# Kernel tuning notes

Hardware: AMD Instinct MI355X
Metric: run time of the kernel (lower is better)

Reference implementation:

```python
import jax, jax.numpy as jnp
import numpy as np

B, S, HID = 4, 1024, 1024
H = 16
D = HID // H  # 64
SPARSITY = 0.9  # keep prob = 0.1


def setup_inputs() -> dict:
    key = jax.random.key(0)
    ks = jax.random.split(key, 11)
    sc = 1.0 / np.sqrt(HID)
    x = jax.random.normal(ks[0], (B, S, HID), dtype=jnp.float32)
    Wq = jax.random.normal(ks[1], (HID, HID), dtype=jnp.float32) * sc
    bq = jnp.zeros((HID,), dtype=jnp.float32)
    Wk = jax.random.normal(ks[2], (HID, HID), dtype=jnp.float32) * sc
    bk = jnp.zeros((HID,), dtype=jnp.float32)
    Wv = jax.random.normal(ks[3], (HID, HID), dtype=jnp.float32) * sc
    bv = jnp.zeros((HID,), dtype=jnp.float32)
    Wo = jax.random.normal(ks[4], (HID, HID), dtype=jnp.float32) * sc
    bo = jnp.zeros((HID,), dtype=jnp.float32)
    temperature = jnp.ones((H, 1, 1), dtype=jnp.float32)
    # training-mode random sparsity mask: rand > sparsity -> keep (True)
    sparse_mask = jax.random.uniform(ks[5], (B, H, S, S)) > SPARSITY
    return {"x": x, "Wq": Wq, "bq": bq, "Wk": Wk, "bk": bk, "Wv": Wv,
            "bv": bv, "Wo": Wo, "bo": bo, "temperature": temperature,
            "sparse_mask": sparse_mask}


def reference(x, Wq, bq, Wk, bk, Wv, bv, Wo, bo, temperature, sparse_mask):
    b, s, _ = x.shape
    def split_heads(t):
        return t.reshape(b, s, H, D).transpose(0, 2, 1, 3)  # [B,H,S,D]
    q = split_heads(x @ Wq + bq)
    k = split_heads(x @ Wk + bk)
    v = split_heads(x @ Wv + bv)
    scores = jnp.einsum('bhqd,bhkd->bhqk', q, k) / np.sqrt(D)
    scores = scores * temperature  # [H,1,1] broadcasts over [B,H,S,S]
    scores = jnp.where(sparse_mask, scores, -jnp.inf)
    attn = jax.nn.softmax(scores, axis=-1)
    out = jnp.einsum('bhqk,bhkd->bhqd', attn, v)
    out = out.transpose(0, 2, 1, 3).reshape(b, s, HID)
    return out @ Wo + bo
```

## Files before the change

### kernel.cpp

```cpp
#include <hip/hip_runtime.h>

typedef unsigned short u16;
typedef short short8 __attribute__((ext_vector_type(8)));
typedef float f32x4 __attribute__((ext_vector_type(4)));
typedef float float4v __attribute__((ext_vector_type(4)));
typedef u16 u16x4 __attribute__((ext_vector_type(4)));
typedef unsigned uint2v __attribute__((ext_vector_type(2)));
typedef unsigned long long u64;

__device__ __forceinline__ u16 f2bf(float f) {
  union { float f; unsigned u; } v; v.f = f;
  unsigned r = v.u + 0x7FFFu + ((v.u >> 16) & 1u);
  return (u16)(r >> 16);
}

__device__ __forceinline__ unsigned cvtpk(float lo, float hi) {
  unsigned r;
  asm("v_cvt_pk_bf16_f32 %0, %1, %2" : "=v"(r) : "v"(lo), "v"(hi));
  return r;
}

__device__ __forceinline__ void gload16(const void* g, void* l) {
  __builtin_amdgcn_global_load_lds(
      (const __attribute__((address_space(1))) void*)g,
      (__attribute__((address_space(3))) void*)l, 16, 0, 0);
}

union PackSS { unsigned u[4]; short8 s; };

__global__ __launch_bounds__(256)
void cvt_kernel(const float* __restrict__ x, u16* __restrict__ xb,
                const float* __restrict__ W0, const float* __restrict__ W1,
                const float* __restrict__ W2, const float* __restrict__ W3,
                u16* __restrict__ Wt) {
  __shared__ float t[32][33];
  const int bid = blockIdx.x;
  if (bid < 4096) {
    int i = (bid * 256 + threadIdx.x) * 4;
    float4v v = *(const float4v*)(x + i);
    u16x4 o;
    o[0] = f2bf(v[0]); o[1] = f2bf(v[1]); o[2] = f2bf(v[2]); o[3] = f2bf(v[3]);
    *(u16x4*)(xb + i) = o;
  } else {
    int i = bid - 4096;
    int z = i >> 10, rest = i & 1023;
    const float* W = (z == 0) ? W0 : (z == 1) ? W1 : (z == 2) ? W2 : W3;
    u16* outw = Wt + (size_t)z * 1048576;
    int n0 = (rest & 31) * 32, k0 = (rest >> 5) * 32;
    int tx = threadIdx.x & 31, ty = threadIdx.x >> 5;
#pragma unroll
    for (int j = 0; j < 4; ++j)
      t[ty + 8 * j][tx] = W[(size_t)(k0 + ty + 8 * j) * 1024 + n0 + tx];
    __syncthreads();
#pragma unroll
    for (int j = 0; j < 4; ++j)
      outw[(size_t)(n0 + ty + 8 * j) * 1024 + k0 + tx] = f2bf(t[tx][ty + 8 * j]);
  }
}

template<int BM, int BN>
__global__ __launch_bounds__(256, 3)
void gemm_kernel(const u16* __restrict__ A,
                 const u16* __restrict__ Bt0, const u16* __restrict__ Bt1, const u16* __restrict__ Bt2,
                 const float* __restrict__ b0, const float* __restrict__ b1, const float* __restrict__ b2,
                 const float* __restrict__ temp,
                 u16* __restrict__ qb, u16* __restrict__ kb, u16* __restrict__ vT,
                 float* __restrict__ fo, int phase,
                 const void* __restrict__ mask, u64* __restrict__ bits) {
  constexpr int K = 1024;
  constexpr int WM = BM / 2;
  constexpr int WN = BN / 2;
  constexpr int MR = WM / 16;
  constexpr int NC = WN / 16;
  __shared__ u16 As[BM * 32];
  __shared__ u16 Bs[BN * 32];
  __shared__ int sf;
  const int tid = threadIdx.x;
  const int lane = tid & 63, w = tid >> 6;
  const int l15 = lane & 15, l4 = lane >> 4;
  const int m0 = blockIdx.x * BM, n0 = blockIdx.y * BN;
  const int z = blockIdx.z;
  const u16* Bt = (z == 0) ? Bt0 : (z == 1) ? Bt1 : Bt2;
  const float* bias = (z == 0) ? b0 : (z == 1) ? b1 : b2;
  const int wr = w >> 1, wc = w & 1;

  f32x4 acc[MR][NC] = {};

  const int c0 = tid, c1 = 256 + tid;
  const u16* ga0 = A + (size_t)(m0 + (c0 >> 2)) * K + (c0 & 3) * 8;
  const u16* ga1 = A + (size_t)(m0 + (c1 >> 2)) * K + (c1 & 3) * 8;
  const u16* gb0 = Bt + (size_t)(n0 + (c0 >> 2)) * K + (c0 & 3) * 8;
  const u16* gb1 = Bt + (size_t)(n0 + (c1 >> 2)) * K + (c1 & 3) * 8;
  u16* la0 = As + c0 * 8;
  u16* la1 = As + c1 * 8;
  u16* lb0 = Bs + c0 * 8;
  u16* lb1 = Bs + c1 * 8;

  for (int kt = 0; kt < K; kt += 32) {
    gload16(ga0 + kt, la0);
    if (BM == 128) gload16(ga1 + kt, la1);
    gload16(gb0 + kt, lb0);
    if (BN == 128) gload16(gb1 + kt, lb1);
    __syncthreads();
    short8 af[MR], bfr[NC];
#pragma unroll
    for (int r = 0; r < MR; ++r)
      af[r] = *(const short8*)(As + (wr * WM + r * 16 + l15) * 32 + l4 * 8);
#pragma unroll
    for (int c = 0; c < NC; ++c)
      bfr[c] = *(const short8*)(Bs + (wc * WN + c * 16 + l15) * 32 + l4 * 8);
#pragma unroll
    for (int r = 0; r < MR; ++r)
#pragma unroll
      for (int c = 0; c < NC; ++c)
        acc[r][c] = __builtin_amdgcn_mfma_f32_16x16x32_bf16(bfr[c], af[r], acc[r][c], 0, 0, 0);
    __syncthreads();
  }

  float bvj[NC][4];
#pragma unroll
  for (int c = 0; c < NC; ++c)
#pragma unroll
    for (int j = 0; j < 4; ++j)
      bvj[c][j] = bias[n0 + wc * WN + c * 16 + l4 * 4 + j];
  const float fac = (phase == 0 && z == 0)
      ? temp[(n0 + wc * WN) >> 6] * 0.18033688011112042f : 1.0f;

#pragma unroll
  for (int r = 0; r < MR; ++r) {
    const int mm = m0 + wr * WM + r * 16 + l15;
    const int b = mm >> 10, s = mm & 1023;
#pragma unroll
    for (int c = 0; c < NC; ++c) {
      const int n = n0 + wc * WN + c * 16 + l4 * 4;
      if (phase == 1) {
        float4v o;
#pragma unroll
        for (int j = 0; j < 4; ++j) o[j] = acc[r][c][j] + bvj[c][j];
        *(float4v*)(fo + (size_t)mm * 1024 + n) = o;
      } else if (z == 2) {
#pragma unroll
        for (int j = 0; j < 4; ++j)
          vT[((size_t)b * 1024 + n + j) * 1024 + s] = f2bf(acc[r][c][j] + bvj[c][j]);
      } else {
        unsigned lo = cvtpk((acc[r][c][0] + bvj[c][0]) * fac, (acc[r][c][1] + bvj[c][1]) * fac);
        unsigned hi = cvtpk((acc[r][c][2] + bvj[c][2]) * fac, (acc[r][c][3] + bvj[c][3]) * fac);
        unsigned o2[2] = {lo, hi};
        int hh = n >> 6, d = n & 63;
        u16* dst = (z == 0) ? qb : kb;
        *(unsigned long long*)(dst + ((((size_t)b * 16 + hh) * 1024 + s) * 64 + d)) =
            *(unsigned long long*)o2;
      }
    }
  }

  if (phase == 0) {
    if (tid == 0) sf = 0;
    __syncthreads();
    {
      uint4 v = ((const uint4*)mask)[tid];
      unsigned xs[4] = {v.x, v.y, v.z, v.w};
      int f = 0;
#pragma unroll
      for (int d = 0; d < 4; ++d) {
        unsigned u = xs[d];
        if (u == 0x3F800000u) f |= 1;
        if (u & 0xFFFFFF00u) f |= 2;
        if ((d & 1) && u) f |= 4;
      }
      if (f) atomicOr(&sf, f);
    }
    __syncthreads();
    const int fl = sf;
    const int fmt = (fl & 1) ? 2 : ((fl & 2) ? 0 : ((fl & 4) ? 1 : 3));

    const int gb = z * 256 + blockIdx.y * 32 + blockIdx.x;
    for (int it = 0; it < 6; ++it) {
      const int wi = (it * 768 + gb) * 256 + tid;
      if (wi >= 1048576) break;
      u64 b = 0;
      if (fmt == 0) {
        const uint4* mp = (const uint4*)mask + (size_t)wi * 4;
#pragma unroll
        for (int i = 0; i < 4; ++i) {
          uint4 v = mp[i];
          unsigned xw[4] = {v.x, v.y, v.z, v.w};
#pragma unroll
          for (int d = 0; d < 4; ++d)
#pragma unroll
            for (int by = 0; by < 4; ++by)
              if (xw[d] & (0xFFu << (by * 8))) b |= 1ULL << (i * 16 + d * 4 + by);
        }
      } else if (fmt != 3) {
        const uint4* mp = (const uint4*)mask + (size_t)wi * 16;
#pragma unroll
        for (int i = 0; i < 16; ++i) {
          uint4 v = mp[i];
          if (v.x) b |= 1ULL << (i * 4 + 0);
          if (v.y) b |= 1ULL << (i * 4 + 1);
          if (v.z) b |= 1ULL << (i * 4 + 2);
          if (v.w) b |= 1ULL << (i * 4 + 3);
        }
      } else {
        const uint4* mp = (const uint4*)mask + (size_t)wi * 32;
#pragma unroll
        for (int i = 0; i < 32; ++i) {
          uint4 v = mp[i];
          if (v.x | v.y) b |= 1ULL << (i * 2 + 0);
          if (v.z | v.w) b |= 1ULL << (i * 2 + 1);
        }
      }
      int bh = wi >> 14, q = (wi >> 4) & 1023, kt = wi & 15;
      bits[((size_t)bh * 16 + kt) * 1024 + q] = b;
    }
  }
}

__device__ __forceinline__ void softmax_reg(f32x4* s, u64 wcur, float& m,
                                            f32x4* oacc, f32x4& lacc, int l4,
                                            PackSS& p0, PackSS& p1) {
  float mt = fmaxf(fmaxf(s[0][0], s[0][1]), fmaxf(s[0][2], s[0][3]));
#pragma unroll
  for (int cb = 1; cb < 4; ++cb)
    mt = fmaxf(mt, fmaxf(fmaxf(s[cb][0], s[cb][1]), fmaxf(s[cb][2], s[cb][3])));
  mt = fmaxf(mt, __shfl_xor(mt, 16));
  mt = fmaxf(mt, __shfl_xor(mt, 32));
  if (!__all(mt <= m + 8.f)) {
    float mnew = fmaxf(m, mt);
    float al = exp2f(m - mnew);
    lacc *= al;
#pragma unroll
    for (int db = 0; db < 4; ++db) oacc[db] *= al;
    m = mnew;
  }
  unsigned hws[4] = {(unsigned)wcur, (unsigned)(wcur >> 16),
                     (unsigned)(wcur >> 32), (unsigned)(wcur >> 48)};
#pragma unroll
  for (int cb = 0; cb < 4; ++cb) {
#pragma unroll
    for (int j = 0; j < 4; ++j) {
      float p = exp2f(s[cb][j] - m);
      s[cb][j] = ((hws[cb] >> (l4 * 4 + j)) & 1) ? p : 0.f;
    }
  }
  p0.u[0] = cvtpk(s[0][0], s[0][1]); p0.u[1] = cvtpk(s[0][2], s[0][3]);
  p0.u[2] = cvtpk(s[1][0], s[1][1]); p0.u[3] = cvtpk(s[1][2], s[1][3]);
  p1.u[0] = cvtpk(s[2][0], s[2][1]); p1.u[1] = cvtpk(s[2][2], s[2][3]);
  p1.u[2] = cvtpk(s[3][0], s[3][1]); p1.u[3] = cvtpk(s[3][2], s[3][3]);
}

__global__ __launch_bounds__(256, 3)
void attn_kernel(const u16* __restrict__ qb, const u16* __restrict__ kb,
                 const u16* __restrict__ vT, const u64* __restrict__ mbits,
                 u16* __restrict__ oh) {
  __shared__ u16 Ks[2][64 * 64];
  __shared__ u16 Vs[2][64 * 64];
  const int tid = threadIdx.x, lane = tid & 63, w = tid >> 6;
  const int l15 = lane & 15, l4 = lane >> 4;
  const int id = blockIdx.x;
  const int xcd = id & 7;
  const int bh = xcd * 8 + ((id >> 3) & 7), qx = id >> 6;
  const int b = bh >> 4, h = bh & 15;
  const int q0 = qx * 128 + w * 32;
  const u16* qp = qb + ((size_t)bh * 1024 + q0) * 64;
  const u16* kp = kb + (size_t)bh * 1024 * 64;
  const u16* vp = vT + (size_t)bh * 64 * 1024;

  const int L0 = tid, L1 = tid + 256;
  const int r0 = L0 >> 3, c0 = ((L0 & 7) ^ (r0 & 7)) * 8;
  const int r1 = L1 >> 3, c1 = ((L1 & 7) ^ (r1 & 7)) * 8;
  const int swz8 = (l15 & 7) << 3;
  const int vswz = l15 & 7;

  int koff[4], vr[4], ke0, ke1, ve[2][2];
#pragma unroll
  for (int cb = 0; cb < 4; ++cb) koff[cb] = (cb * 16 + l15) * 64;
#pragma unroll
  for (int db = 0; db < 4; ++db) vr[db] = (db * 16 + l15) * 64;
  ke0 = (l4 * 8) ^ swz8;
  ke1 = (32 + l4 * 8) ^ swz8;
#pragma unroll
  for (int kg = 0; kg < 2; ++kg) {
    ve[kg][0] = (((4 * kg + (l4 >> 1)) ^ vswz) << 3) + (l4 & 1) * 4;
    ve[kg][1] = (((4 * kg + 2 + (l4 >> 1)) ^ vswz) << 3) + (l4 & 1) * 4;
  }

  short8 qa0 = *(const short8*)(qp + (size_t)l15 * 64 + l4 * 8);
  short8 qa1 = *(const short8*)(qp + (size_t)l15 * 64 + 32 + l4 * 8);
  short8 qb0 = *(const short8*)(qp + (size_t)(16 + l15) * 64 + l4 * 8);
  short8 qb1 = *(const short8*)(qp + (size_t)(16 + l15) * 64 + 32 + l4 * 8);

  PackSS ones;
  ones.u[0] = 0x3F803F80u; ones.u[1] = 0x3F803F80u;
  ones.u[2] = 0x3F803F80u; ones.u[3] = 0x3F803F80u;

  float mA = -1e30f, mB = -1e30f;
  f32x4 oA[4] = {}, oB[4] = {};
  f32x4 lA4 = {}, lB4 = {};

  const u64* mb = mbits + (size_t)bh * 16 * 1024 + q0 + l15;
  u64 wA = mb[0], wB = mb[16];

  gload16(kp + (size_t)r0 * 64 + c0, &Ks[0][L0 * 8]);
  gload16(kp + (size_t)r1 * 64 + c1, &Ks[0][L1 * 8]);
  gload16(vp + (size_t)r0 * 1024 + c0, &Vs[0][L0 * 8]);
  gload16(vp + (size_t)r1 * 1024 + c1, &Vs[0][L1 * 8]);

  for (int t = 0; t < 16; ++t) {
    const int buf = t & 1;
    __syncthreads();

    if (t < 15) {
      const int k1 = (t + 1) * 64;
      gload16(kp + (size_t)(k1 + r0) * 64 + c0, &Ks[buf ^ 1][L0 * 8]);
      gload16(kp + (size_t)(k1 + r1) * 64 + c1, &Ks[buf ^ 1][L1 * 8]);
      gload16(vp + (size_t)r0 * 1024 + k1 + c0, &Vs[buf ^ 1][L0 * 8]);
      gload16(vp + (size_t)r1 * 1024 + k1 + c1, &Vs[buf ^ 1][L1 * 8]);
    }
    u64 wAn = 0, wBn = 0;
    if (t < 15) { wAn = mb[(t + 1) * 1024]; wBn = mb[(t + 1) * 1024 + 16]; }

    const u16* kbase = Ks[buf];
    f32x4 sa[4] = {}, sb[4] = {};
    __builtin_amdgcn_s_setprio(1);
#pragma unroll
    for (int cb = 0; cb < 4; ++cb) {
      short8 kf0 = *(const short8*)(kbase + koff[cb] + ke0);
      short8 kf1 = *(const short8*)(kbase + koff[cb] + ke1);
      sa[cb] = __builtin_amdgcn_mfma_f32_16x16x32_bf16(kf0, qa0, sa[cb], 0, 0, 0);
      sa[cb] = __builtin_amdgcn_mfma_f32_16x16x32_bf16(kf1, qa1, sa[cb], 0, 0, 0);
      sb[cb] = __builtin_amdgcn_mfma_f32_16x16x32_bf16(kf0, qb0, sb[cb], 0, 0, 0);
      sb[cb] = __builtin_amdgcn_mfma_f32_16x16x32_bf16(kf1, qb1, sb[cb], 0, 0, 0);
    }
    __builtin_amdgcn_s_setprio(0);

    PackSS pa0, pa1, pb0, pb1;
    softmax_reg(sa, wA, mA, oA, lA4, l4, pa0, pa1);
    softmax_reg(sb, wB, mB, oB, lB4, l4, pb0, pb1);

    const u16* vbase = Vs[buf];
    __builtin_amdgcn_s_setprio(1);
#pragma unroll
    for (int kg = 0; kg < 2; ++kg) {
#pragma unroll
      for (int db = 0; db < 4; ++db) {
        uint2v v0 = *(const uint2v*)(vbase + vr[db] + ve[kg][0]);
        uint2v v1 = *(const uint2v*)(vbase + vr[db] + ve[kg][1]);
        PackSS vf;
        vf.u[0] = v0[0]; vf.u[1] = v0[1]; vf.u[2] = v1[0]; vf.u[3] = v1[1];
        oA[db] = __builtin_amdgcn_mfma_f32_16x16x32_bf16(
            vf.s, kg ? pa1.s : pa0.s, oA[db], 0, 0, 0);
        oB[db] = __builtin_amdgcn_mfma_f32_16x16x32_bf16(
            vf.s, kg ? pb1.s : pb0.s, oB[db], 0, 0, 0);
      }
      lA4 = __builtin_amdgcn_mfma_f32_16x16x32_bf16(
          ones.s, kg ? pa1.s : pa0.s, lA4, 0, 0, 0);
      lB4 = __builtin_amdgcn_mfma_f32_16x16x32_bf16(
          ones.s, kg ? pb1.s : pb0.s, lB4, 0, 0, 0);
    }
    __builtin_amdgcn_s_setprio(0);
    wA = wAn; wB = wBn;
  }

  float rlA = 1.f / lA4[0], rlB = 1.f / lB4[0];
  u16* orowA = oh + ((size_t)b * 1024 + q0 + l15) * 1024 + h * 64;
  u16* orowB = oh + ((size_t)b * 1024 + q0 + 16 + l15) * 1024 + h * 64;
#pragma unroll
  for (int db = 0; db < 4; ++db) {
    unsigned a0 = cvtpk(oA[db][0] * rlA, oA[db][1] * rlA);
    unsigned a1 = cvtpk(oA[db][2] * rlA, oA[db][3] * rlA);
    unsigned b0 = cvtpk(oB[db][0] * rlB, oB[db][1] * rlB);
    unsigned b1 = cvtpk(oB[db][2] * rlB, oB[db][3] * rlB);
    unsigned oAa[2] = {a0, a1}, oBb[2] = {b0, b1};
    *(unsigned long long*)(orowA + db * 16 + l4 * 4) = *(unsigned long long*)oAa;
    *(unsigned long long*)(orowB + db * 16 + l4 * 4) = *(unsigned long long*)oBb;
  }
}

extern "C" void kernel_launch(void* const* d_in, const int* in_sizes, int n_in,
                              void* d_out, int out_size, void* d_ws, size_t ws_size,
                              hipStream_t stream) {
  const float* x = (const float*)d_in[0];
  const float* Wq = (const float*)d_in[1];
  const float* bq = (const float*)d_in[2];
  const float* Wk = (const float*)d_in[3];
  const float* bk = (const float*)d_in[4];
  const float* Wv = (const float*)d_in[5];
  const float* bv = (const float*)d_in[6];
  const float* Wo = (const float*)d_in[7];
  const float* bo = (const float*)d_in[8];
  const float* temp = (const float*)d_in[9];
  const void* mask = (const void*)d_in[10];

  char* ws = (char*)d_ws;
  u16* xb = (u16*)(ws + 256);
  u16* Wt = xb + (size_t)4 * 1024 * 1024;
  u16* qbuf = Wt + (size_t)4 * 1024 * 1024;
  u16* kbuf = qbuf + (size_t)4 * 1024 * 1024;
  u16* vTb = kbuf + (size_t)4 * 1024 * 1024;
  u64* mbits = (u64*)(vTb + (size_t)4 * 1024 * 1024);
  u16* oh = xb;

  cvt_kernel<<<8192, 256, 0, stream>>>(x, xb, Wq, Wk, Wv, Wo, Wt);
  gemm_kernel<128, 128><<<dim3(32, 8, 3), 256, 0, stream>>>(
      xb, Wt, Wt + 1048576, Wt + 2 * 1048576,
      bq, bk, bv, temp, qbuf, kbuf, vTb, nullptr, 0, mask, mbits);
  attn_kernel<<<512, 256, 0, stream>>>(qbuf, kbuf, vTb, mbits, oh);
  gemm_kernel<64, 64><<<dim3(64, 16, 1), 256, 0, stream>>>(
      oh, Wt + 3 * 1048576, nullptr, nullptr,
      bo, nullptr, nullptr, temp, nullptr, nullptr, nullptr,
      (float*)d_out, 1, nullptr, nullptr);
}
```

Measured before the change: 164.4 us.

## Stagger two query sub-tiles' softmax and PV MFMAs, preload K/V fragments into registers

The inner loop now loads all K and V fragments from LDS into registers up front. It then interleaves work across the two 16-row query sub-tiles: softmax for A, PV for A, softmax for B, PV for B. This is meant to let the VALU-heavy softmax of one sub-tile overlap with the MFMA work of the other, and to hide LDS latency. Holding the extra fragments raises register pressure, so launch bounds drop from 3 to 2 blocks per SM, trading occupancy for instruction-level overlap.

```diff
diff --git a/kernel.cpp b/kernel.cpp
--- a/kernel.cpp
+++ b/kernel.cpp
@@ -249,7 +249,7 @@
   p1.u[2] = cvtpk(s[3][0], s[3][1]); p1.u[3] = cvtpk(s[3][2], s[3][3]);
 }
 
-__global__ __launch_bounds__(256, 3)
+__global__ __launch_bounds__(256, 2)
 void attn_kernel(const u16* __restrict__ qb, const u16* __restrict__ kb,
                  const u16* __restrict__ vT, const u64* __restrict__ mbits,
                  u16* __restrict__ oh) {
@@ -321,40 +321,64 @@
     if (t < 15) { wAn = mb[(t + 1) * 1024]; wBn = mb[(t + 1) * 1024 + 16]; }
 
     const u16* kbase = Ks[buf];
+    short8 kfr[8];
+#pragma unroll
+    for (int cb = 0; cb < 4; ++cb) {
+      kfr[2 * cb]     = *(const short8*)(kbase + koff[cb] + ke0);
+      kfr[2 * cb + 1] = *(const short8*)(kbase + koff[cb] + ke1);
+    }
+
     f32x4 sa[4] = {}, sb[4] = {};
     __builtin_amdgcn_s_setprio(1);
 #pragma unroll
     for (int cb = 0; cb < 4; ++cb) {
-      short8 kf0 = *(const short8*)(kbase + koff[cb] + ke0);
-      short8 kf1 = *(const short8*)(kbase + koff[cb] + ke1);
-      sa[cb] = __builtin_amdgcn_mfma_f32_16x16x32_bf16(kf0, qa0, sa[cb], 0, 0, 0);
-      sa[cb] = __builtin_amdgcn_mfma_f32_16x16x32_bf16(kf1, qa1, sa[cb], 0, 0, 0);
-      sb[cb] = __builtin_amdgcn_mfma_f32_16x16x32_bf16(kf0, qb0, sb[cb], 0, 0, 0);
-      sb[cb] = __builtin_amdgcn_mfma_f32_16x16x32_bf16(kf1, qb1, sb[cb], 0, 0, 0);
+      sa[cb] = __builtin_amdgcn_mfma_f32_16x16x32_bf16(kfr[2 * cb], qa0, sa[cb], 0, 0, 0);
+      sa[cb] = __builtin_amdgcn_mfma_f32_16x16x32_bf16(kfr[2 * cb + 1], qa1, sa[cb], 0, 0, 0);
+    }
+#pragma unroll
+    for (int cb = 0; cb < 4; ++cb) {
+      sb[cb] = __builtin_amdgcn_mfma_f32_16x16x32_bf16(kfr[2 * cb], qb0, sb[cb], 0, 0, 0);
+      sb[cb] = __builtin_amdgcn_mfma_f32_16x16x32_bf16(kfr[2 * cb + 1], qb1, sb[cb], 0, 0, 0);
     }
     __builtin_amdgcn_s_setprio(0);
 
-    PackSS pa0, pa1, pb0, pb1;
+    PackSS pa0, pa1;
     softmax_reg(sa, wA, mA, oA, lA4, l4, pa0, pa1);
-    softmax_reg(sb, wB, mB, oB, lB4, l4, pb0, pb1);
 
     const u16* vbase = Vs[buf];
-    __builtin_amdgcn_s_setprio(1);
-#pragma unroll
-    for (int kg = 0; kg < 2; ++kg) {
+    PackSS vfr[2][4];
+#pragma unroll
+    for (int kg = 0; kg < 2; ++kg)
 #pragma unroll
       for (int db = 0; db < 4; ++db) {
         uint2v v0 = *(const uint2v*)(vbase + vr[db] + ve[kg][0]);
         uint2v v1 = *(const uint2v*)(vbase + vr[db] + ve[kg][1]);
-        PackSS vf;
-        vf.u[0] = v0[0]; vf.u[1] = v0[1]; vf.u[2] = v1[0]; vf.u[3] = v1[1];
+        vfr[kg][db].u[0] = v0[0]; vfr[kg][db].u[1] = v0[1];
+        vfr[kg][db].u[2] = v1[0]; vfr[kg][db].u[3] = v1[1];
+      }
+
+    __builtin_amdgcn_s_setprio(1);
+#pragma unroll
+    for (int kg = 0; kg < 2; ++kg) {
+#pragma unroll
+      for (int db = 0; db < 4; ++db)
         oA[db] = __builtin_amdgcn_mfma_f32_16x16x32_bf16(
-            vf.s, kg ? pa1.s : pa0.s, oA[db], 0, 0, 0);
-        oB[db] = __builtin_amdgcn_mfma_f32_16x16x32_bf16(
-            vf.s, kg ? pb1.s : pb0.s, oB[db], 0, 0, 0);
-      }
+            vfr[kg][db].s, kg ? pa1.s : pa0.s, oA[db], 0, 0, 0);
       lA4 = __builtin_amdgcn_mfma_f32_16x16x32_bf16(
           ones.s, kg ? pa1.s : pa0.s, lA4, 0, 0, 0);
+    }
+    __builtin_amdgcn_s_setprio(0);
+
+    PackSS pb0, pb1;
+    softmax_reg(sb, wB, mB, oB, lB4, l4, pb0, pb1);
+
+    __builtin_amdgcn_s_setprio(1);
+#pragma unroll
+    for (int kg = 0; kg < 2; ++kg) {
+#pragma unroll
+      for (int db = 0; db < 4; ++db)
+        oB[db] = __builtin_amdgcn_mfma_f32_16x16x32_bf16(
+            vfr[kg][db].s, kg ? pb1.s : pb0.s, oB[db], 0, 0, 0);
       lB4 = __builtin_amdgcn_mfma_f32_16x16x32_bf16(
           ones.s, kg ? pb1.s : pb0.s, lB4, 0, 0, 0);
     }
```

Result: no change. 165.8 us (+0.9%).
